# Optimization experiments

Hardware: AMD Instinct MI355X
Metric: run time of the kernel (lower is better)

## Reference

```python
import jax, jax.numpy as jnp
import numpy as np
import math

B, L, DIM, S = 4, 4096, 2048, 128


def setup_inputs() -> dict:
    key = jax.random.key(0)
    ks = jax.random.split(key, 10)
    n_fast = int(S * 0.4)
    n_med = int(S * 0.3)
    n_slow = S - n_fast - n_med
    # multi-timescale eigenvalue init (fast/medium/slow lanes), as in the module
    log_A_real = jnp.concatenate([
        jnp.linspace(math.log(0.9), math.log(0.99), n_fast),
        jnp.linspace(math.log(0.999), math.log(0.9999), n_med),
        jnp.linspace(math.log(0.99999), math.log(0.999999), n_slow),
    ]).astype(jnp.float32)
    log_A_imag = jnp.linspace(0.001, math.pi, S).astype(jnp.float32)

    def rn(k, sh, sc):
        return jax.random.normal(k, sh, jnp.float32) * sc

    return {
        "x": jax.random.normal(ks[0], (B, L, DIM, 2), jnp.float32),
        "log_A_real": log_A_real,
        "log_A_imag": log_A_imag,
        "D": rn(ks[1], (DIM, 2), 0.01),
        "dt_w": rn(ks[2], (S, 2 * DIM), (2 * DIM) ** -0.5),   # dt_proj weight (out,in)
        "dt_b": jnp.zeros((S,), jnp.float32),                  # dt_proj bias
        "dt_bias": jnp.full((S,), -4.0, jnp.float32),          # extra dt_bias param
        "Br": rn(ks[3], (DIM, S), DIM ** -0.5),                # B_proj real weight (in,out)
        "Bi": rn(ks[4], (DIM, S), DIM ** -0.5),                # B_proj imag weight
        "Cr": rn(ks[5], (S, DIM), S ** -0.5),                  # C_proj real weight (in,out)
        "Ci": rn(ks[6], (S, DIM), S ** -0.5),                  # C_proj imag weight
        "pg_w": rn(ks[7], (S, DIM), DIM ** -0.5),              # protect_gate weight (out,in)
        "pg_b": jnp.full((S,), -3.0, jnp.float32),             # protect_gate bias (init -3)
    }


def _combine(left, right):
    # associative op for h[t] = a[t]*h[t-1] + b[t]: (a1,b1) o (a2,b2) = (a1*a2, a2*b1 + b2)
    a1, b1 = left
    a2, b2 = right
    return a1 * a2, a2 * b1 + b2


def reference(x, log_A_real, log_A_imag, D, dt_w, dt_b, dt_bias, Br, Bi, Cr, Ci, pg_w, pg_b):
    xr, xi = x[..., 0], x[..., 1]                     # (B,L,dim) each
    xc = jax.lax.complex(xr, xi)                      # complex input
    x_flat = jnp.concatenate([xr, xi], axis=-1)       # to_real(x, 'concat') -> (B,L,2*dim)
    dt = jax.nn.softplus(x_flat @ dt_w.T + dt_b + dt_bias)   # (B,L,S)
    A_mag = jnp.exp(-dt * jnp.exp(log_A_real))                # (B,L,S)
    eig = jax.lax.complex(jnp.cos(log_A_imag), jnp.sin(log_A_imag))  # unit-circle phase (S,)
    A = A_mag * eig                                           # complex transition (B,L,S)
    Bx = (xc @ jax.lax.complex(Br, Bi)) * dt                  # complex B_proj(x) * dt
    # GSP: gated state protection -> interpolate toward identity dynamics
    cab = jnp.sqrt(xr * xr + xi * xi)                         # cabs(x) (B,L,dim)
    protect = jax.nn.sigmoid(cab @ pg_w.T + pg_b)             # (B,L,S)
    A = protect.astype(A.dtype) + (1.0 - protect) * A         # protect*I + (1-p)*A
    Bx = (1.0 - protect) * Bx
    # parallel prefix scan over time axis
    h = jax.lax.associative_scan(_combine, (A, Bx), axis=1)[1]  # (B,L,S) complex
    y = h @ jax.lax.complex(Cr, Ci)                           # C_proj(h) -> (B,L,dim) complex
    y = y + jax.lax.complex(D[:, 0], D[:, 1]) * xc            # D skip: cmul(D, x)
    y_out = jnp.stack([jnp.real(y), jnp.imag(y)], axis=-1)    # (B,L,dim,2)
    h_last = jnp.stack([jnp.real(h[:, -1]), jnp.imag(h[:, -1])], axis=-1)  # (B,S,2)
    return y_out, h_last
```

## Files before the change

kernel.cpp:

```cpp
#include <hip/hip_runtime.h>
#include <math.h>

#define BB   4
#define LL   4096
#define DIMC 2048
#define SC   128
#define MM   (BB*LL)
#define NC   256
#define LCH  (LL/NC)

typedef __attribute__((ext_vector_type(8))) short bf16x8;
typedef __attribute__((ext_vector_type(4))) float f32x4;

#define MFMA(a,b,c) __builtin_amdgcn_mfma_f32_16x16x32_bf16(a,b,c,0,0,0)

__device__ inline unsigned short bf16h(float v) {
    unsigned u = __float_as_uint(v);
    return (unsigned short)((u + 0x7FFFu + ((u >> 16) & 1u)) >> 16);
}
__device__ inline float bf2f(unsigned short h) {
    return __uint_as_float(((unsigned)h) << 16);
}

#define W1_SLOTS (128*24)
#define W2_SLOTS (64*8)
#define W3_SLOTS (8*256)
__global__ void prep_w(const float* __restrict__ dt_w,
                       const float* __restrict__ Br,
                       const float* __restrict__ Bi,
                       const float* __restrict__ pg_w,
                       const float* __restrict__ Cr,
                       const float* __restrict__ Ci,
                       short* __restrict__ W1h, short* __restrict__ W1l,
                       short* __restrict__ W2h, short* __restrict__ W2l,
                       short* __restrict__ W3h, short* __restrict__ W3l) {
    int id = threadIdx.x + blockIdx.x * 256;
    int lane = id & 63;
    int slot = id >> 6;
    float v[8];
    short* dsth; short* dstl;
    if (slot < W1_SLOTS) {
        int kt = slot / 24, nf = slot % 24;
        int n  = nf * 16 + (lane & 15);
        int k0 = kt * 32 + 8 * (lane >> 4);
        if (n < 128) {
            const float* p = dt_w + (size_t)n * 4096 + k0;
            #pragma unroll
            for (int j = 0; j < 8; ++j) v[j] = p[j];
        } else if (n < 256) {
            int s = n - 128;
            #pragma unroll
            for (int j = 0; j < 8; ++j) {
                int k = k0 + j;
                v[j] = (k < 2048) ? Br[(size_t)k * 128 + s]
                                  : -Bi[(size_t)(k - 2048) * 128 + s];
            }
        } else {
            int s = n - 256;
            #pragma unroll
            for (int j = 0; j < 8; ++j) {
                int k = k0 + j;
                v[j] = (k < 2048) ? Bi[(size_t)k * 128 + s]
                                  : Br[(size_t)(k - 2048) * 128 + s];
            }
        }
        dsth = W1h + (size_t)id * 8; dstl = W1l + (size_t)id * 8;
    } else if (slot < W1_SLOTS + W2_SLOTS) {
        int s2 = slot - W1_SLOTS;
        int kt = s2 / 8, nf = s2 % 8;
        int s  = nf * 16 + (lane & 15);
        int k0 = kt * 32 + 8 * (lane >> 4);
        const float* p = pg_w + (size_t)s * 2048 + k0;
        #pragma unroll
        for (int j = 0; j < 8; ++j) v[j] = p[j];
        dsth = W2h + (size_t)(id - W1_SLOTS * 64) * 8;
        dstl = W2l + (size_t)(id - W1_SLOTS * 64) * 8;
    } else {
        int s3 = slot - W1_SLOTS - W2_SLOTS;
        int kt = s3 / 256, nf = s3 % 256;
        int n  = nf * 16 + (lane & 15);
        int d = n >> 1, comp = n & 1;
        int k0 = kt * 32 + 8 * (lane >> 4);
        #pragma unroll
        for (int j = 0; j < 8; ++j) {
            int k = k0 + j;
            int s = k & 127;
            float c;
            if (k < 128) c = comp ? Ci[(size_t)s * 2048 + d] : Cr[(size_t)s * 2048 + d];
            else         c = comp ? Cr[(size_t)s * 2048 + d] : -Ci[(size_t)s * 2048 + d];
            v[j] = c;
        }
        dsth = W3h + (size_t)(id - (W1_SLOTS + W2_SLOTS) * 64) * 8;
        dstl = W3l + (size_t)(id - (W1_SLOTS + W2_SLOTS) * 64) * 8;
    }
    bf16x8 hv, lv;
    #pragma unroll
    for (int j = 0; j < 8; ++j) {
        unsigned short h = bf16h(v[j]);
        hv[j] = (short)h;
        lv[j] = (short)bf16h(v[j] - bf2f(h));
    }
    *(bf16x8*)dsth = hv;
    *(bf16x8*)dstl = lv;
}

__global__ __launch_bounds__(512, 2) void phase1(
    const float* __restrict__ x,
    const short* __restrict__ W1h, const short* __restrict__ W1l,
    const short* __restrict__ W2h, const short* __restrict__ W2l,
    const float* __restrict__ log_A_real,
    const float* __restrict__ log_A_imag,
    const float* __restrict__ dt_b,
    const float* __restrict__ dt_bias,
    const float* __restrict__ pg_b,
    float* __restrict__ ABx)
{
    const int tid  = threadIdx.x;
    const int lane = tid & 63;
    const int wv   = tid >> 6;
    const int m0   = blockIdx.x * 64;

    __shared__ __align__(16) union SmemT {
        short comp[6][2][4][64][8];
        float ep[32][512];
    } smem;

    f32x4 c1[3][4];
    f32x4 c2[4];
    #pragma unroll
    for (int n = 0; n < 3; ++n)
        #pragma unroll
        for (int m = 0; m < 4; ++m) c1[n][m] = (f32x4){0.f,0.f,0.f,0.f};
    #pragma unroll
    for (int m = 0; m < 4; ++m) c2[m] = (f32x4){0.f,0.f,0.f,0.f};

    const float2* x2 = (const float2*)x;
    const int srow = tid >> 3;
    const int sdg  = tid & 7;
    const int smf  = srow >> 4;
    const int skf  = sdg >> 2;
    const int spl  = (srow & 15) + 16 * (sdg & 3);

    float4 q[4];
    {
        const float4* xp = (const float4*)(x2 + (size_t)(m0 + srow) * DIMC + sdg * 8);
        #pragma unroll
        for (int i = 0; i < 4; ++i) q[i] = xp[i];
    }

    for (int db = 0; db < 32; ++db) {
        __syncthreads();
        {
            bf16x8 vxh, vxl, vih, vil, vch, vcl;
            #pragma unroll
            for (int j = 0; j < 8; ++j) {
                int qi = j >> 1;
                float xr = (j & 1) ? q[qi].z : q[qi].x;
                float xi = (j & 1) ? q[qi].w : q[qi].y;
                unsigned short h1 = bf16h(xr);
                vxh[j] = (short)h1; vxl[j] = (short)bf16h(xr - bf2f(h1));
                unsigned short h2 = bf16h(xi);
                vih[j] = (short)h2; vil[j] = (short)bf16h(xi - bf2f(h2));
                float cb = sqrtf(fmaf(xr, xr, xi * xi));
                unsigned short h3 = bf16h(cb);
                vch[j] = (short)h3; vcl[j] = (short)bf16h(cb - bf2f(h3));
            }
            *(bf16x8*)&smem.comp[0][skf][smf][spl][0] = vxh;
            *(bf16x8*)&smem.comp[1][skf][smf][spl][0] = vxl;
            *(bf16x8*)&smem.comp[2][skf][smf][spl][0] = vih;
            *(bf16x8*)&smem.comp[3][skf][smf][spl][0] = vil;
            *(bf16x8*)&smem.comp[4][skf][smf][spl][0] = vch;
            *(bf16x8*)&smem.comp[5][skf][smf][spl][0] = vcl;
        }
        __syncthreads();
        if (db < 31) {
            const float4* xp = (const float4*)(x2 + (size_t)(m0 + srow) * DIMC
                                               + (db + 1) * 64 + sdg * 8);
            #pragma unroll
            for (int i = 0; i < 4; ++i) q[i] = xp[i];
        }
        const int KTb = db * 2;
        #pragma unroll
        for (int kf = 0; kf < 2; ++kf) {
            bf16x8 ah[4], al[4];
            #pragma unroll
            for (int mf = 0; mf < 4; ++mf) {
                ah[mf] = *(const bf16x8*)&smem.comp[0][kf][mf][lane][0];
                al[mf] = *(const bf16x8*)&smem.comp[1][kf][mf][lane][0];
            }
            {
                size_t base = ((size_t)(KTb + kf) * 24 + wv * 3) * 64 + lane;
                const bf16x8* bh_p = (const bf16x8*)W1h + base;
                const bf16x8* bl_p = (const bf16x8*)W1l + base;
                #pragma unroll
                for (int nf = 0; nf < 3; ++nf) {
                    bf16x8 bh = bh_p[nf * 64], bl = bl_p[nf * 64];
                    #pragma unroll
                    for (int mf = 0; mf < 4; ++mf) {
                        f32x4 c = c1[nf][mf];
                        c = MFMA(ah[mf], bh, c);
                        c = MFMA(ah[mf], bl, c);
                        c = MFMA(al[mf], bh, c);
                        c1[nf][mf] = c;
                    }
                }
            }
            #pragma unroll
            for (int mf = 0; mf < 4; ++mf) {
                ah[mf] = *(const bf16x8*)&smem.comp[2][kf][mf][lane][0];
                al[mf] = *(const bf16x8*)&smem.comp[3][kf][mf][lane][0];
            }
            {
                size_t base = ((size_t)(64 + KTb + kf) * 24 + wv * 3) * 64 + lane;
                const bf16x8* bh_p = (const bf16x8*)W1h + base;
                const bf16x8* bl_p = (const bf16x8*)W1l + base;
                #pragma unroll
                for (int nf = 0; nf < 3; ++nf) {
                    bf16x8 bh = bh_p[nf * 64], bl = bl_p[nf * 64];
                    #pragma unroll
                    for (int mf = 0; mf < 4; ++mf) {
                        f32x4 c = c1[nf][mf];
                        c = MFMA(ah[mf], bh, c);
                        c = MFMA(ah[mf], bl, c);
                        c = MFMA(al[mf], bh, c);
                        c1[nf][mf] = c;
                    }
                }
            }
            #pragma unroll
            for (int mf = 0; mf < 4; ++mf) {
                ah[mf] = *(const bf16x8*)&smem.comp[4][kf][mf][lane][0];
                al[mf] = *(const bf16x8*)&smem.comp[5][kf][mf][lane][0];
            }
            {
                size_t base = ((size_t)(KTb + kf) * 8 + wv) * 64 + lane;
                bf16x8 bh = ((const bf16x8*)W2h)[base];
                bf16x8 bl = ((const bf16x8*)W2l)[base];
                #pragma unroll
                for (int mf = 0; mf < 4; ++mf) {
                    f32x4 c = c2[mf];
                    c = MFMA(ah[mf], bh, c);
                    c = MFMA(ah[mf], bl, c);
                    c = MFMA(al[mf], bh, c);
                    c2[mf] = c;
                }
            }
        }
    }
    __syncthreads();

    float* ep = &smem.ep[0][0];
    const int es = tid & 127;
    const int eq = tid >> 7;
    float eAr  = expf(log_A_real[es]);
    float egr  = cosf(log_A_imag[es]);
    float egi  = sinf(log_A_imag[es]);
    float bsum = dt_b[es] + dt_bias[es];
    float pgb  = pg_b[es];
    float4* AB4 = (float4*)ABx;

    #pragma unroll
    for (int half = 0; half < 2; ++half) {
        #pragma unroll
        for (int mfh = 0; mfh < 2; ++mfh) {
            int mf = half * 2 + mfh;
            int rl = mfh * 16 + (lane >> 4) * 4;
            #pragma unroll
            for (int nf = 0; nf < 3; ++nf) {
                f32x4 c = c1[nf][mf];
                int col = wv * 48 + nf * 16 + (lane & 15);
                #pragma unroll
                for (int r = 0; r < 4; ++r) ep[(rl + r) * 512 + col] = c[r];
            }
            {
                f32x4 c = c2[mf];
                int col = 384 + wv * 16 + (lane & 15);
                #pragma unroll
                for (int r = 0; r < 4; ++r) ep[(rl + r) * 512 + col] = c[r];
            }
        }
        __syncthreads();
        #pragma unroll
        for (int i = 0; i < 8; ++i) {
            int rl = eq + i * 4;
            float zd   = ep[rl * 512 + es]       + bsum;
            float abr  = ep[rl * 512 + 128 + es];
            float abi  = ep[rl * 512 + 256 + es];
            float zp   = ep[rl * 512 + 384 + es] + pgb;
            float dt   = fmaxf(zd, 0.f) + log1pf(expf(-fabsf(zd)));
            float amag = expf(-dt * eAr);
            float pr   = 1.f / (1.f + expf(-zp));
            float omp  = 1.f - pr;
            float Ar_  = fmaf(omp, amag * egr, pr);
            float Ai_  = omp * amag * egi;
            float sc   = omp * dt;
            AB4[(size_t)(m0 + half * 32 + rl) * SC + es] =
                make_float4(Ar_, Ai_, sc * abr, sc * abi);
        }
        __syncthreads();
    }
}

__global__ void scan_reduce(const float* __restrict__ ABx,
                            float* __restrict__ aggAB) {
    int s = threadIdx.x;
    int c = blockIdx.x & (NC-1);
    int b = blockIdx.x >> 8;
    const float4* AB4 = (const float4*)ABx;
    size_t base = ((size_t)(b * LL + c * LCH) * SC + s);
    float4 v = AB4[base];
    float ar = v.x, ai = v.y, br = v.z, bi = v.w;
    #pragma unroll
    for (int t = 1; t < LCH; ++t) {
        float4 u = AB4[base + (size_t)t * SC];
        float nar = ar*u.x - ai*u.y;
        float nai = ar*u.y + ai*u.x;
        float nbr = br*u.x - bi*u.y + u.z;
        float nbi = br*u.y + bi*u.x + u.w;
        ar = nar; ai = nai; br = nbr; bi = nbi;
    }
    ((float4*)aggAB)[(size_t)blockIdx.x * SC + s] = make_float4(ar, ai, br, bi);
}

__global__ void scan_spine(const float* __restrict__ aggAB,
                           float* __restrict__ preB) {
    int t = threadIdx.x + blockIdx.x * blockDim.x;
    int s = t & 127, b = t >> 7;
    const float4* A4 = (const float4*)aggAB;
    float2* P2 = (float2*)preB;
    float pa_r = 1.f, pa_i = 0.f, pb_r = 0.f, pb_i = 0.f;
    for (int c = 0; c < NC; ++c) {
        size_t idx = (size_t)(b * NC + c) * SC + s;
        P2[idx] = make_float2(pb_r, pb_i);
        float4 a = A4[idx];
        float nar = pa_r*a.x - pa_i*a.y;
        float nai = pa_r*a.y + pa_i*a.x;
        float nbr = pb_r*a.x - pb_i*a.y + a.z;
        float nbi = pb_r*a.y + pb_i*a.x + a.w;
        pa_r = nar; pa_i = nai; pb_r = nbr; pb_i = nbi;
    }
}

__global__ void scan_apply(float* __restrict__ ABx,
                           const float* __restrict__ preB,
                           float* __restrict__ d_out) {
    int s = threadIdx.x;
    int c = blockIdx.x & (NC-1);
    int b = blockIdx.x >> 8;
    float4* AB4 = (float4*)ABx;
    float2 hp = ((const float2*)preB)[(size_t)blockIdx.x * SC + s];
    float hr = hp.x, hi = hp.y;
    size_t base = ((size_t)(b * LL + c * LCH) * SC + s);
    #pragma unroll
    for (int t = 0; t < LCH; ++t) {
        size_t idx = base + (size_t)t * SC;
        float4 u = AB4[idx];
        float nr = u.x*hr - u.y*hi + u.z;
        float ni = u.x*hi + u.y*hr + u.w;
        hr = nr; hi = ni;
        ((float2*)&AB4[idx])[0] = make_float2(hr, hi);
    }
    if (c == NC - 1) {
        float2* hl = (float2*)(d_out + (size_t)MM * DIMC * 2);
        hl[b * SC + s] = make_float2(hr, hi);
    }
}

__global__ __launch_bounds__(512, 6) void phase3(
    const float* __restrict__ ABx,
    const short* __restrict__ W3h, const short* __restrict__ W3l,
    const float* __restrict__ x,
    const float* __restrict__ Dw,
    float* __restrict__ out)
{
    const int tid  = threadIdx.x;
    const int lane = tid & 63;
    const int wv   = tid >> 6;
    const int bn   = blockIdx.x & 7;
    const int bm   = blockIdx.x >> 3;
    const int m0   = bm * 32;

    __shared__ __align__(16) short ldsA[2][8][2][64][8];

    {
        int row = tid >> 4, sg = tid & 15;
        int mf = row >> 4, r15 = row & 15;
        int kfr = sg >> 2, lg = sg & 3;
        int pl = r15 + 16 * lg;
        const float4* hp = (const float4*)ABx + (size_t)(m0 + row) * SC + sg * 8;
        bf16x8 rh, rl, ih, il;
        #pragma unroll
        for (int j = 0; j < 8; ++j) {
            float4 u = hp[j];
            unsigned short h1 = bf16h(u.x);
            rh[j] = (short)h1; rl[j] = (short)bf16h(u.x - bf2f(h1));
            unsigned short h2 = bf16h(u.y);
            ih[j] = (short)h2; il[j] = (short)bf16h(u.y - bf2f(h2));
        }
        *(bf16x8*)&ldsA[0][kfr][mf][pl][0]     = rh;
        *(bf16x8*)&ldsA[1][kfr][mf][pl][0]     = rl;
        *(bf16x8*)&ldsA[0][kfr + 4][mf][pl][0] = ih;
        *(bf16x8*)&ldsA[1][kfr + 4][mf][pl][0] = il;
    }
    __syncthreads();

    f32x4 c[4][2];
    #pragma unroll
    for (int n = 0; n < 4; ++n)
        #pragma unroll
        for (int m = 0; m < 2; ++m) c[n][m] = (f32x4){0.f,0.f,0.f,0.f};

    #pragma unroll
    for (int kf = 0; kf < 8; ++kf) {
        bf16x8 ah[2], al[2];
        #pragma unroll
        for (int mf = 0; mf < 2; ++mf) {
            ah[mf] = *(const bf16x8*)&ldsA[0][kf][mf][lane][0];
            al[mf] = *(const bf16x8*)&ldsA[1][kf][mf][lane][0];
        }
        size_t base = ((size_t)kf * 256 + bn * 32 + wv * 4) * 64 + lane;
        const bf16x8* bh_p = (const bf16x8*)W3h + base;
        const bf16x8* bl_p = (const bf16x8*)W3l + base;
        #pragma unroll
        for (int nf = 0; nf < 4; ++nf) {
            bf16x8 bh = bh_p[nf * 64], bl = bl_p[nf * 64];
            #pragma unroll
            for (int mf = 0; mf < 2; ++mf) {
                f32x4 cc = c[nf][mf];
                cc = MFMA(ah[mf], bh, cc);
                cc = MFMA(ah[mf], bl, cc);
                cc = MFMA(al[mf], bh, cc);
                c[nf][mf] = cc;
            }
        }
    }

    const float2* x2  = (const float2*)x;
    const float2* Dw2 = (const float2*)Dw;
    #pragma unroll
    for (int nf = 0; nf < 4; ++nf) {
        int n = bn * 512 + wv * 64 + nf * 16 + (lane & 15);
        int d = n >> 1, comp = n & 1;
        float2 dw = Dw2[d];
        #pragma unroll
        for (int mf = 0; mf < 2; ++mf) {
            f32x4 cc = c[nf][mf];
            int mbase = m0 + mf * 16 + (lane >> 4) * 4;
            #pragma unroll
            for (int r = 0; r < 4; ++r) {
                int m = mbase + r;
                float2 xv = x2[(size_t)m * DIMC + d];
                float val = cc[r] + (comp ? fmaf(dw.x, xv.y,  dw.y * xv.x)
                                          : fmaf(dw.x, xv.x, -dw.y * xv.y));
                out[(size_t)m * 4096 + n] = val;
            }
        }
    }
}

extern "C" void kernel_launch(void* const* d_in, const int* in_sizes, int n_in,
                              void* d_out, int out_size, void* d_ws, size_t ws_size,
                              hipStream_t stream) {
    const float* x          = (const float*)d_in[0];
    const float* log_A_real = (const float*)d_in[1];
    const float* log_A_imag = (const float*)d_in[2];
    const float* Dw         = (const float*)d_in[3];
    const float* dt_w       = (const float*)d_in[4];
    const float* dt_b       = (const float*)d_in[5];
    const float* dt_bias    = (const float*)d_in[6];
    const float* Br         = (const float*)d_in[7];
    const float* Bi         = (const float*)d_in[8];
    const float* Cr         = (const float*)d_in[9];
    const float* Ci         = (const float*)d_in[10];
    const float* pg_w       = (const float*)d_in[11];
    const float* pg_b       = (const float*)d_in[12];

    float* out = (float*)d_out;
    float* ws  = (float*)d_ws;

    short* W1h = (short*)ws;
    short* W1l = W1h + (size_t)W1_SLOTS * 64 * 8;
    short* W2h = W1l + (size_t)W1_SLOTS * 64 * 8;
    short* W2l = W2h + (size_t)W2_SLOTS * 64 * 8;
    float* aggAB = ws + 1835008;
    float* preB  = aggAB + (size_t)BB * NC * SC * 4;
    float* ABx   = ws + 2621440;
    short* W3h   = (short*)(ws + 2621440 + 8388608);
    short* W3l   = W3h + (size_t)W3_SLOTS * 64 * 8;

    hipLaunchKernelGGL(prep_w, dim3((W1_SLOTS+W2_SLOTS+W3_SLOTS)*64/256), dim3(256), 0, stream,
                       dt_w, Br, Bi, pg_w, Cr, Ci, W1h, W1l, W2h, W2l, W3h, W3l);
    hipLaunchKernelGGL(phase1, dim3(MM/64), dim3(512), 0, stream,
                       x, W1h, W1l, W2h, W2l, log_A_real, log_A_imag,
                       dt_b, dt_bias, pg_b, ABx);
    hipLaunchKernelGGL(scan_reduce, dim3(BB*NC), dim3(128), 0, stream,
                       ABx, aggAB);
    hipLaunchKernelGGL(scan_spine, dim3(2), dim3(256), 0, stream,
                       aggAB, preB);
    hipLaunchKernelGGL(scan_apply, dim3(BB*NC), dim3(128), 0, stream,
                       ABx, preB, out);
    hipLaunchKernelGGL(phase3, dim3(4096), dim3(512), 0, stream,
                       ABx, W3h, W3l, x, Dw, out);
}
```

Baseline: 945.0 us.

## Shrink phase1 epilogue staging buffer and raise occupancy hint

The epilogue of phase1 now stages one 16-row MFMA fragment at a time in a padded 16x520 LDS buffer instead of two 32x512 halves. This lowers the kernel's shared-memory footprint to allow more resident blocks, and the launch bounds now ask for 6 blocks per CU. The padding is meant to reduce LDS bank conflicts. In exchange there are more barriers in the epilogue, and the tighter register budget implied by the higher occupancy hint may cause spills of the accumulator registers.

```diff
diff --git a/kernel.cpp b/kernel.cpp
--- a/kernel.cpp
+++ b/kernel.cpp
@@ -104,7 +104,7 @@
     *(bf16x8*)dstl = lv;
 }
 
-__global__ __launch_bounds__(512, 2) void phase1(
+__global__ __launch_bounds__(512, 6) void phase1(
     const float* __restrict__ x,
     const short* __restrict__ W1h, const short* __restrict__ W1l,
     const short* __restrict__ W2h, const short* __restrict__ W2l,
@@ -122,7 +122,7 @@
 
     __shared__ __align__(16) union SmemT {
         short comp[6][2][4][64][8];
-        float ep[32][512];
+        float ep[16][520];
     } smem;
 
     f32x4 c1[3][4];
@@ -247,9 +247,7 @@
             }
         }
     }
-    __syncthreads();
-
-    float* ep = &smem.ep[0][0];
+
     const int es = tid & 127;
     const int eq = tid >> 7;
     float eAr  = expf(log_A_real[es]);
@@ -260,33 +258,32 @@
     float4* AB4 = (float4*)ABx;
 
     #pragma unroll
-    for (int half = 0; half < 2; ++half) {
-        #pragma unroll
-        for (int mfh = 0; mfh < 2; ++mfh) {
-            int mf = half * 2 + mfh;
-            int rl = mfh * 16 + (lane >> 4) * 4;
+    for (int mf = 0; mf < 4; ++mf) {
+        __syncthreads();
+        {
+            int rb   = (lane >> 4) * 4;
+            int colA = wv * 48 + (lane & 15);
             #pragma unroll
             for (int nf = 0; nf < 3; ++nf) {
                 f32x4 c = c1[nf][mf];
-                int col = wv * 48 + nf * 16 + (lane & 15);
                 #pragma unroll
-                for (int r = 0; r < 4; ++r) ep[(rl + r) * 512 + col] = c[r];
-            }
-            {
-                f32x4 c = c2[mf];
-                int col = 384 + wv * 16 + (lane & 15);
-                #pragma unroll
-                for (int r = 0; r < 4; ++r) ep[(rl + r) * 512 + col] = c[r];
-            }
+                for (int r = 0; r < 4; ++r)
+                    smem.ep[rb + r][colA + nf * 16] = c[r];
+            }
+            f32x4 c = c2[mf];
+            int colB = 384 + wv * 16 + (lane & 15);
+            #pragma unroll
+            for (int r = 0; r < 4; ++r)
+                smem.ep[rb + r][colB] = c[r];
         }
         __syncthreads();
         #pragma unroll
-        for (int i = 0; i < 8; ++i) {
-            int rl = eq + i * 4;
-            float zd   = ep[rl * 512 + es]       + bsum;
-            float abr  = ep[rl * 512 + 128 + es];
-            float abi  = ep[rl * 512 + 256 + es];
-            float zp   = ep[rl * 512 + 384 + es] + pgb;
+        for (int i = 0; i < 4; ++i) {
+            int rl = eq * 4 + i;
+            float zd   = smem.ep[rl][es]       + bsum;
+            float abr  = smem.ep[rl][128 + es];
+            float abi  = smem.ep[rl][256 + es];
+            float zp   = smem.ep[rl][384 + es] + pgb;
             float dt   = fmaxf(zd, 0.f) + log1pf(expf(-fabsf(zd)));
             float amag = expf(-dt * eAr);
             float pr   = 1.f / (1.f + expf(-zp));
@@ -294,10 +291,9 @@
             float Ar_  = fmaf(omp, amag * egr, pr);
             float Ai_  = omp * amag * egi;
             float sc   = omp * dt;
-            AB4[(size_t)(m0 + half * 32 + rl) * SC + es] =
+            AB4[(size_t)(m0 + mf * 16 + rl) * SC + es] =
                 make_float4(Ar_, Ai_, sc * abr, sc * abi);
         }
-        __syncthreads();
     }
 }
 
```

After: 1.735 ms. 1.84x slower.
